# Kernel tuning notes

Hardware: AMD Instinct MI355X
Metric: run time of the kernel (lower is better)

Reference implementation:

```python
import jax, jax.numpy as jnp
import numpy as np

DEPTH, DIM, HEADS, EXP = 6, 768, 12, 4
B, N = 8, 1024
EPS = 1e-5


def setup_inputs() -> dict:
    key = jax.random.key(0)
    ks = jax.random.split(key, 6)
    s = 0.02
    inp = {
        "x": jax.random.normal(ks[0], (B, N, DIM), dtype=jnp.float32),
        "ln1_g": jnp.ones((DEPTH, DIM), jnp.float32),
        "ln1_b": jnp.zeros((DEPTH, DIM), jnp.float32),
        "wqkv": jax.random.normal(ks[1], (DEPTH, DIM, 3 * DIM), jnp.float32) * s,
        "bqkv": jnp.zeros((DEPTH, 3 * DIM), jnp.float32),
        "ln2_g": jnp.ones((DEPTH, DIM), jnp.float32),
        "ln2_b": jnp.zeros((DEPTH, DIM), jnp.float32),
        "w1": jax.random.normal(ks[2], (DEPTH, DIM, EXP * DIM), jnp.float32) * s,
        "b1": jnp.zeros((DEPTH, EXP * DIM), jnp.float32),
        "w2": jax.random.normal(ks[3], (DEPTH, EXP * DIM, DIM), jnp.float32) * s,
        "b2": jnp.zeros((DEPTH, DIM), jnp.float32),
    }
    return inp


def _layernorm(x, g, b):
    mu = jnp.mean(x, axis=-1, keepdims=True)
    var = jnp.mean(jnp.square(x - mu), axis=-1, keepdims=True)
    return (x - mu) * jax.lax.rsqrt(var + EPS) * g + b


def _block(x, p):
    ln1_g, ln1_b, wqkv, bqkv, ln2_g, ln2_b, w1, b1, w2, b2 = p
    # --- attention (pre-norm, residual) ---
    x1 = _layernorm(x, ln1_g, ln1_b)
    qkv = x1 @ wqkv + bqkv  # [b, n, 3*dim]
    q, k, v = jnp.split(qkv, 3, axis=-1)
    dh = DIM // HEADS
    def heads(t):  # b n (h d) -> b h n d
        return t.reshape(B, N, HEADS, dh).transpose(0, 2, 1, 3)
    q, k, v = heads(q), heads(k), heads(v)
    scale = DIM ** (-0.5)  # NB: module scales by full dim, not head dim
    dots = jnp.einsum("bhnd,bhmd->bhnm", q, k) * scale
    attn = jax.nn.softmax(dots, axis=-1)
    out = jnp.einsum("bhnm,bhmd->bhnd", attn, v)
    out = out.transpose(0, 2, 1, 3).reshape(B, N, DIM)
    x = x + out
    # --- feedforward (pre-norm, residual) ---
    x2 = _layernorm(x, ln2_g, ln2_b)
    h = jax.nn.gelu(x2 @ w1 + b1, approximate=False)
    x = x + (h @ w2 + b2)
    return x


def reference(x, ln1_g, ln1_b, wqkv, bqkv, ln2_g, ln2_b, w1, b1, w2, b2):
    params = (ln1_g, ln1_b, wqkv, bqkv, ln2_g, ln2_b, w1, b1, w2, b2)

    def body(carry, p):
        return _block(carry, p), None

    x, _ = jax.lax.scan(body, x, params)
    return x
```

## Files before the change

### kernel.cpp

```cpp
#include <hip/hip_runtime.h>
#include <hip/hip_bf16.h>
#include <math.h>

#define DEPTH 6
#define DIM   768
#define HEADS 12
#define DH    64
#define NCTX  1024
#define BATCH 8
#define ROWS  (BATCH*NCTX)
#define DIM3  (3*DIM)
#define DIMF  (4*DIM)
#define LNEPS 1e-5f

typedef __attribute__((ext_vector_type(8)))  short short8;
typedef __attribute__((ext_vector_type(4)))  float floatx4;
typedef __attribute__((ext_vector_type(16))) float floatx16;
using bf16 = __hip_bfloat16;
typedef unsigned int u32;

static __device__ __forceinline__ bf16 f2bf(float v){ return __float2bfloat16(v); }
static __device__ __forceinline__ float bf2f(unsigned short u){
    union { unsigned int i; float f; } c; c.i = ((unsigned int)u) << 16; return c.f;
}
static __device__ __forceinline__ unsigned short bfu(float v){ return __bfloat16_as_ushort(f2bf(v)); }
static __device__ __forceinline__ u32 pk2(float a, float b){
    return (u32)bfu(a) | ((u32)bfu(b) << 16);
}

static __device__ __forceinline__ void gl_lds16(const void* g, void* l) {
    __builtin_amdgcn_global_load_lds((const __attribute__((address_space(1))) void*)g,
                                     (__attribute__((address_space(3))) void*)l, 16, 0, 0);
}

__global__ void k_transpose_convert(const float* __restrict__ W, bf16* __restrict__ WT,
                                    int K, int N) {
    __shared__ float tile[32][33];
    int l = blockIdx.z;
    const float* Wl = W + (size_t)l * K * N;
    bf16* WTl = WT + (size_t)l * K * N;
    int n0 = blockIdx.x * 32, k0 = blockIdx.y * 32;
    int tx = threadIdx.x, ty = threadIdx.y;
#pragma unroll
    for (int i = 0; i < 4; i++)
        tile[ty + i*8][tx] = Wl[(size_t)(k0 + ty + i*8) * N + n0 + tx];
    __syncthreads();
#pragma unroll
    for (int i = 0; i < 4; i++)
        WTl[(size_t)(n0 + ty + i*8) * K + k0 + tx] = f2bf(tile[tx][ty + i*8]);
}

__global__ __launch_bounds__(256) void k_layernorm(const float* __restrict__ x,
                                                   const float* __restrict__ g,
                                                   const float* __restrict__ b,
                                                   bf16* __restrict__ y) {
    int row  = blockIdx.x * 4 + (threadIdx.x >> 6);
    int lane = threadIdx.x & 63;
    const float4* xr = (const float4*)(x + (size_t)row * DIM);
    float4 v[3];
    float s = 0.f, s2 = 0.f;
#pragma unroll
    for (int i = 0; i < 3; i++) {
        v[i] = xr[lane + i*64];
        s  += v[i].x + v[i].y + v[i].z + v[i].w;
        s2 += v[i].x*v[i].x + v[i].y*v[i].y + v[i].z*v[i].z + v[i].w*v[i].w;
    }
#pragma unroll
    for (int m = 1; m < 64; m <<= 1) { s += __shfl_xor(s, m); s2 += __shfl_xor(s2, m); }
    float mu  = s * (1.f / DIM);
    float var = s2 * (1.f / DIM) - mu * mu;
    float rs  = rsqrtf(var + LNEPS);
    bf16* yr = y + (size_t)row * DIM;
    const float4* g4 = (const float4*)g;
    const float4* b4 = (const float4*)b;
#pragma unroll
    for (int i = 0; i < 3; i++) {
        float4 gg = g4[lane + i*64], bb = b4[lane + i*64];
        float r0 = (v[i].x - mu) * rs * gg.x + bb.x;
        float r1 = (v[i].y - mu) * rs * gg.y + bb.y;
        float r2 = (v[i].z - mu) * rs * gg.z + bb.z;
        float r3 = (v[i].w - mu) * rs * gg.w + bb.w;
        uint2 u; u.x = pk2(r0, r1); u.y = pk2(r2, r3);
        *(uint2*)&yr[4 * (lane + i*64)] = u;
    }
}

template<int MODE, int BN>
__global__ __launch_bounds__(256) void k_gemm(const bf16* __restrict__ A,
                                              const bf16* __restrict__ WT,
                                              const float* __restrict__ bias,
                                              bf16* __restrict__ outb,
                                              float* __restrict__ outf,
                                              int N, int K) {
    constexpr int JF = BN / 32;
    __shared__ __align__(16) bf16 As[3][128*32];
    __shared__ __align__(16) bf16 Bs[3][BN*32];
    int nt = N / BN;
    int nwg = gridDim.x;
    int fblk = blockIdx.x;
    int swz = (fblk & 7) * (nwg >> 3) + (fblk >> 3);
    int m0 = (swz / nt) * 128, n0 = (swz % nt) * BN;
    int t = threadIdx.x;
    int lane = t & 63, w = t >> 6;
    int wr = (w >> 1) * 64, wc = (w & 1) * (BN / 2);
    int lr = lane & 15, lg = lane >> 4;
    int c0 = t, c1 = 256 + t;
    int r0g = c0 >> 2, e0 = (c0 & 3) * 8;
    int r1g = c1 >> 2, e1 = (c1 & 3) * 8;
    const bf16* Arow0 = A  + (size_t)(m0 + r0g) * K + e0;
    const bf16* Arow1 = A  + (size_t)(m0 + r1g) * K + e1;
    const bf16* Brow0 = WT + (size_t)(n0 + r0g) * K + e0;
    const bf16* Brow1 = WT + (size_t)(n0 + r1g) * K + e1;

    floatx4 acc[4][JF] = {};
    int NT = K >> 5;

    auto STAGE = [&](int ks, int buf) {
        int ko = ks << 5;
        gl_lds16(Arow0 + ko, &As[buf][c0 * 8]);
        gl_lds16(Arow1 + ko, &As[buf][c1 * 8]);
        gl_lds16(Brow0 + ko, &Bs[buf][c0 * 8]);
        if constexpr (BN == 128) gl_lds16(Brow1 + ko, &Bs[buf][c1 * 8]);
    };

    STAGE(0, 0);
    STAGE(1, 1);
    if constexpr (BN == 128) asm volatile("s_waitcnt vmcnt(4)" ::: "memory");
    else                     asm volatile("s_waitcnt vmcnt(3)" ::: "memory");
    __builtin_amdgcn_s_barrier();

    for (int kb = 0; kb < NT; kb += 3) {
#pragma unroll
        for (int s = 0; s < 3; s++) {
            int ks = kb + s;
            bool pf = (ks + 2) < NT;
            if (pf) STAGE(ks + 2, (s + 2) % 3);
            short8 af[4], bfr[JF];
#pragma unroll
            for (int i = 0; i < 4; i++)  af[i]  = *(const short8*)&As[s][(wr + i*16 + lr)*32 + lg*8];
#pragma unroll
            for (int j = 0; j < JF; j++) bfr[j] = *(const short8*)&Bs[s][(wc + j*16 + lr)*32 + lg*8];
#pragma unroll
            for (int i = 0; i < 4; i++)
#pragma unroll
                for (int j = 0; j < JF; j++)
                    acc[i][j] = __builtin_amdgcn_mfma_f32_16x16x32_bf16(af[i], bfr[j], acc[i][j], 0, 0, 0);
            if (pf) {
                if constexpr (BN == 128) asm volatile("s_waitcnt vmcnt(4)" ::: "memory");
                else                     asm volatile("s_waitcnt vmcnt(3)" ::: "memory");
            } else {
                asm volatile("s_waitcnt vmcnt(0)" ::: "memory");
            }
            __builtin_amdgcn_s_barrier();
        }
    }
#pragma unroll
    for (int i = 0; i < 4; i++)
#pragma unroll
        for (int j = 0; j < JF; j++)
#pragma unroll
            for (int r = 0; r < 4; r++) {
                int row = m0 + wr + i*16 + lg*4 + r;
                int col = n0 + wc + j*16 + lr;
                float vv = acc[i][j][r] + bias[col];
                if (MODE == 0) {
                    outb[(size_t)row * N + col] = f2bf(vv);
                } else if (MODE == 1) {
                    float u = 1.5957691216f * (vv + 0.044715f * vv * vv * vv);
                    float gs = 1.f / (1.f + __expf(-u));
                    outb[(size_t)row * N + col] = f2bf(vv * gs);
                } else {
                    outf[(size_t)row * N + col] += vv;
                }
            }
}

static __device__ __forceinline__ int vt_off(int d, int k) {
    int dw = d * 36 + (k >> 1);
    dw ^= (d & 0x38) >> 1;
    return dw * 2 + (k & 1);
}

__global__ __launch_bounds__(256, 3) void k_attn(const bf16* __restrict__ qkv,
                                                 float* __restrict__ x) {
    int f = blockIdx.x;
    int b  = f & 7;
    int rr = f >> 3;
    int h  = rr % 12;
    int qt = rr / 12;
    int t = threadIdx.x, lane = t & 63, w = t >> 6;
    int q = lane & 31, hi = lane >> 5;
    const size_t bn0 = (size_t)b * NCTX;
    const bf16* Qg = qkv + bn0 * DIM3 + h * DH;
    const bf16* Kg = Qg + DIM;
    const bf16* Vg = Qg + 2 * DIM;
    int q0 = qt * 128 + w * 32;

    const float qs = 0.036084391824351615f * 1.4426950408889634f;
    short8 qf[4];
#pragma unroll
    for (int s = 0; s < 4; s++) {
        short8 raw = *(const short8*)&Qg[(size_t)(q0 + q) * DIM3 + s*16 + hi*8];
        short8 o;
#pragma unroll
        for (int e = 0; e < 8; e++)
            o[e] = (short)bfu(bf2f((unsigned short)raw[e]) * qs);
        qf[s] = o;
    }

    __shared__ __align__(16) bf16 KsS[64*64];
    __shared__ __align__(16) bf16 VTs[64*72];
    __shared__ __align__(16) bf16 PsS[4][32*64];
    __shared__ float wbc[4][32];

    u32* ksw = (u32*)KsS;
    u32* psw = (u32*)&PsS[w][0];

    int sr[2], sc[2];
#pragma unroll
    for (int it = 0; it < 2; it++) { int c = it*256 + t; sr[it] = c >> 3; sc[it] = (c & 7) * 8; }

    floatx16 pacc[2] = {};
    float mrow = -3e38f, lrow = 0.f;

    uint4 kreg[2], vreg[2];
#pragma unroll
    for (int it = 0; it < 2; it++) {
        kreg[it] = *(const uint4*)&Kg[(size_t)sr[it] * DIM3 + sc[it]];
        vreg[it] = *(const uint4*)&Vg[(size_t)sr[it] * DIM3 + sc[it]];
    }

    for (int kt = 0; kt < 16; kt++) {
        __syncthreads();
#pragma unroll
        for (int it = 0; it < 2; it++) {
            int row = sr[it], u = sc[it] >> 3;
            *(uint4*)(ksw + row*32 + ((u ^ (row & 7)) << 2)) = kreg[it];
            const bf16* vp = (const bf16*)&vreg[it];
#pragma unroll
            for (int e = 0; e < 8; e++) VTs[vt_off(sc[it] + e, row)] = vp[e];
        }
        __syncthreads();
        if (kt + 1 < 16) {
            int kv0 = (kt + 1) * 64;
#pragma unroll
            for (int it = 0; it < 2; it++) {
                kreg[it] = *(const uint4*)&Kg[(size_t)(kv0 + sr[it]) * DIM3 + sc[it]];
                vreg[it] = *(const uint4*)&Vg[(size_t)(kv0 + sr[it]) * DIM3 + sc[it]];
            }
        }

        floatx16 sacc[2] = {};
#pragma unroll
        for (int kb = 0; kb < 2; kb++) {
#pragma unroll
            for (int s = 0; s < 4; s++) {
                int row = kb*32 + q;
                short8 kf = *(const short8*)(ksw + row*32 + (((2*s + hi) ^ (row & 7)) << 2));
                sacc[kb] = __builtin_amdgcn_mfma_f32_32x32x16_bf16(kf, qf[s], sacc[kb], 0, 0, 0);
            }
        }

        float mx = sacc[0][0];
#pragma unroll
        for (int r = 1; r < 16; r++) mx = fmaxf(mx, sacc[0][r]);
#pragma unroll
        for (int r = 0; r < 16; r++) mx = fmaxf(mx, sacc[1][r]);
        mx = fmaxf(mx, __shfl_xor(mx, 32));
        bool chg = mx > mrow + 8.f;
        if (__any(chg)) {
            float mnew = chg ? mx : mrow;
            float corr = exp2f(mrow - mnew);
            mrow = mnew;
            lrow *= corr;
            wbc[w][q] = corr;
#pragma unroll
            for (int r = 0; r < 16; r++) {
                float c = wbc[w][(r & 3) + 8*(r >> 2) + 4*hi];
                pacc[0][r] *= c; pacc[1][r] *= c;
            }
        }
        float sum = 0.f;
#pragma unroll
        for (int kb = 0; kb < 2; kb++) {
#pragma unroll
            for (int m = 0; m < 4; m++) {
                float p0 = exp2f(sacc[kb][4*m+0] - mrow);
                float p1 = exp2f(sacc[kb][4*m+1] - mrow);
                float p2 = exp2f(sacc[kb][4*m+2] - mrow);
                float p3 = exp2f(sacc[kb][4*m+3] - mrow);
                sum += (p0 + p1) + (p2 + p3);
                uint2 d2; d2.x = pk2(p0, p1); d2.y = pk2(p2, p3);
                *(uint2*)(psw + q*32 + (((m + 4*kb) ^ (q & 7)) << 2) + 2*hi) = d2;
            }
        }
        sum += __shfl_xor(sum, 32);
        lrow += sum;

#pragma unroll
        for (int ks = 0; ks < 4; ks++) {
            short8 pa = *(const short8*)(psw + q*32 + (((2*ks + hi) ^ (q & 7)) << 2));
#pragma unroll
            for (int db = 0; db < 2; db++) {
                short8 vb = *(const short8*)&VTs[vt_off(db*32 + q, 16*ks + 8*hi)];
                pacc[db] = __builtin_amdgcn_mfma_f32_32x32x16_bf16(pa, vb, pacc[db], 0, 0, 0);
            }
        }
    }

    wbc[w][q] = 1.f / lrow;
    float* xr = x + bn0 * DIM + (size_t)h * DH;
#pragma unroll
    for (int r = 0; r < 16; r++) {
        int qrow = (r & 3) + 8*(r >> 2) + 4*hi;
        float li = wbc[w][qrow];
#pragma unroll
        for (int db = 0; db < 2; db++) {
            int col = db*32 + q;
            xr[(size_t)(q0 + qrow) * DIM + col] += pacc[db][r] * li;
        }
    }
}

extern "C" void kernel_launch(void* const* d_in, const int* in_sizes, int n_in,
                              void* d_out, int out_size, void* d_ws, size_t ws_size,
                              hipStream_t stream) {
    const float* x_in  = (const float*)d_in[0];
    const float* ln1_g = (const float*)d_in[1];
    const float* ln1_b = (const float*)d_in[2];
    const float* wqkv  = (const float*)d_in[3];
    const float* bqkv  = (const float*)d_in[4];
    const float* ln2_g = (const float*)d_in[5];
    const float* ln2_b = (const float*)d_in[6];
    const float* w1    = (const float*)d_in[7];
    const float* b1    = (const float*)d_in[8];
    const float* w2    = (const float*)d_in[9];
    const float* b2    = (const float*)d_in[10];
    float* x = (float*)d_out;

    char* ws = (char*)d_ws;
    size_t off = 0;
    auto alloc = [&](size_t bytes) { void* p = ws + off; off += (bytes + 255) & ~255ull; return p; };
    bf16* wqkvT = (bf16*)alloc((size_t)DEPTH * DIM * DIM3 * 2);
    bf16* w1T   = (bf16*)alloc((size_t)DEPTH * DIM * DIMF * 2);
    bf16* w2T   = (bf16*)alloc((size_t)DEPTH * DIMF * DIM * 2);
    bf16* xn    = (bf16*)alloc((size_t)ROWS * DIM * 2);
    bf16* qkvh  = (bf16*)alloc((size_t)ROWS * DIMF * 2);
    if (off > ws_size) return;

    hipMemcpyAsync(x, x_in, (size_t)ROWS * DIM * 4, hipMemcpyDeviceToDevice, stream);

    k_transpose_convert<<<dim3(DIM3/32, DIM/32,  DEPTH), dim3(32, 8), 0, stream>>>(wqkv, wqkvT, DIM,  DIM3);
    k_transpose_convert<<<dim3(DIMF/32, DIM/32,  DEPTH), dim3(32, 8), 0, stream>>>(w1,   w1T,   DIM,  DIMF);
    k_transpose_convert<<<dim3(DIM/32,  DIMF/32, DEPTH), dim3(32, 8), 0, stream>>>(w2,   w2T,   DIMF, DIM);

    for (int l = 0; l < DEPTH; l++) {
        k_layernorm<<<ROWS/4, 256, 0, stream>>>(x, ln1_g + l*DIM, ln1_b + l*DIM, xn);
        k_gemm<0,128><<<dim3((DIM3/128)*(ROWS/128)), 256, 0, stream>>>(
            xn, wqkvT + (size_t)l*DIM*DIM3, bqkv + (size_t)l*DIM3, qkvh, nullptr, DIM3, DIM);
        k_attn<<<dim3(768), 256, 0, stream>>>(qkvh, x);
        k_layernorm<<<ROWS/4, 256, 0, stream>>>(x, ln2_g + l*DIM, ln2_b + l*DIM, xn);
        k_gemm<1,128><<<dim3((DIMF/128)*(ROWS/128)), 256, 0, stream>>>(
            xn, w1T + (size_t)l*DIM*DIMF, b1 + (size_t)l*DIMF, qkvh, nullptr, DIMF, DIM);
        k_gemm<2,64><<<dim3((DIM/64)*(ROWS/128)), 256, 0, stream>>>(
            qkvh, w2T + (size_t)l*DIMF*DIM, b2 + (size_t)l*DIM, nullptr, x, DIM, DIMF);
    }
}
```

Measured before the change: 1.621 ms.

## Deepen GEMM LDS pipeline to five stages with register-fragment double buffering

The GEMM main loop goes from a 3-buffer LDS ring with prefetch distance 2 to a 5-buffer ring with prefetch distance 4. It also double-buffers the MFMA operand fragments in registers, so the LDS reads for the next k-step overlap the current MFMAs. The aim is to hide more global-memory and LDS latency behind matrix math. The cost is more LDS per block, which can lower occupancy, and more live registers. The fixed vmcnt wait counts in the tail iterations may not cover every outstanding stage.

```diff
diff --git a/kernel.cpp b/kernel.cpp
--- a/kernel.cpp
+++ b/kernel.cpp
@@ -92,9 +92,9 @@
                                               bf16* __restrict__ outb,
                                               float* __restrict__ outf,
                                               int N, int K) {
-    constexpr int JF = BN / 32;
-    __shared__ __align__(16) bf16 As[3][128*32];
-    __shared__ __align__(16) bf16 Bs[3][BN*32];
+    constexpr int JF  = BN / 32;
+    __shared__ __align__(16) bf16 As[5][128*32];
+    __shared__ __align__(16) bf16 Bs[5][BN*32];
     int nt = N / BN;
     int nwg = gridDim.x;
     int fblk = blockIdx.x;
@@ -115,45 +115,55 @@
     floatx4 acc[4][JF] = {};
     int NT = K >> 5;
 
-    auto STAGE = [&](int ks, int buf) {
+    auto STAGE = [&](int ks) {
+        int buf = ks % 5;
         int ko = ks << 5;
         gl_lds16(Arow0 + ko, &As[buf][c0 * 8]);
         gl_lds16(Arow1 + ko, &As[buf][c1 * 8]);
         gl_lds16(Brow0 + ko, &Bs[buf][c0 * 8]);
         if constexpr (BN == 128) gl_lds16(Brow1 + ko, &Bs[buf][c1 * 8]);
     };
-
-    STAGE(0, 0);
-    STAGE(1, 1);
-    if constexpr (BN == 128) asm volatile("s_waitcnt vmcnt(4)" ::: "memory");
-    else                     asm volatile("s_waitcnt vmcnt(3)" ::: "memory");
+    auto WAITC = [&]() {
+        if constexpr (BN == 128) asm volatile("s_waitcnt vmcnt(8)" ::: "memory");
+        else                     asm volatile("s_waitcnt vmcnt(6)" ::: "memory");
+    };
+    auto LOADF = [&](int ks, short8* af, short8* bfr) {
+        int buf = ks % 5;
+#pragma unroll
+        for (int i = 0; i < 4; i++)  af[i]  = *(const short8*)&As[buf][(wr + i*16 + lr)*32 + lg*8];
+#pragma unroll
+        for (int j = 0; j < JF; j++) bfr[j] = *(const short8*)&Bs[buf][(wc + j*16 + lr)*32 + lg*8];
+    };
+    auto MFMAC = [&](short8* af, short8* bfr) {
+#pragma unroll
+        for (int i = 0; i < 4; i++)
+#pragma unroll
+            for (int j = 0; j < JF; j++)
+                acc[i][j] = __builtin_amdgcn_mfma_f32_16x16x32_bf16(af[i], bfr[j], acc[i][j], 0, 0, 0);
+    };
+
+    STAGE(0); STAGE(1); STAGE(2); STAGE(3);
+    WAITC();
     __builtin_amdgcn_s_barrier();
-
-    for (int kb = 0; kb < NT; kb += 3) {
-#pragma unroll
-        for (int s = 0; s < 3; s++) {
-            int ks = kb + s;
-            bool pf = (ks + 2) < NT;
-            if (pf) STAGE(ks + 2, (s + 2) % 3);
-            short8 af[4], bfr[JF];
-#pragma unroll
-            for (int i = 0; i < 4; i++)  af[i]  = *(const short8*)&As[s][(wr + i*16 + lr)*32 + lg*8];
-#pragma unroll
-            for (int j = 0; j < JF; j++) bfr[j] = *(const short8*)&Bs[s][(wc + j*16 + lr)*32 + lg*8];
-#pragma unroll
-            for (int i = 0; i < 4; i++)
-#pragma unroll
-                for (int j = 0; j < JF; j++)
-                    acc[i][j] = __builtin_amdgcn_mfma_f32_16x16x32_bf16(af[i], bfr[j], acc[i][j], 0, 0, 0);
-            if (pf) {
-                if constexpr (BN == 128) asm volatile("s_waitcnt vmcnt(4)" ::: "memory");
-                else                     asm volatile("s_waitcnt vmcnt(3)" ::: "memory");
-            } else {
-                asm volatile("s_waitcnt vmcnt(0)" ::: "memory");
-            }
-            __builtin_amdgcn_s_barrier();
-        }
-    }
+    short8 a0[4], b0[JF], a1[4], b1[JF];
+    LOADF(0, a0, b0);
+
+    for (int ks = 0; ks < NT; ks += 2) {
+        if (ks + 4 < NT) STAGE(ks + 4);
+        LOADF(ks + 1, a1, b1);
+        MFMAC(a0, b0);
+        if (ks + 2 < NT) WAITC();
+        else             asm volatile("s_waitcnt vmcnt(0)" ::: "memory");
+        __builtin_amdgcn_s_barrier();
+        int k1 = ks + 1;
+        if (k1 + 4 < NT) STAGE(k1 + 4);
+        if (k1 + 1 < NT) LOADF(k1 + 1, a0, b0);
+        MFMAC(a1, b1);
+        if (k1 + 2 < NT) WAITC();
+        else             asm volatile("s_waitcnt vmcnt(0)" ::: "memory");
+        __builtin_amdgcn_s_barrier();
+    }
+
 #pragma unroll
     for (int i = 0; i < 4; i++)
 #pragma unroll
```

Result: slower. 1.915 ms (+18.1%).
